# Kernel tuning notes

Hardware: AMD Instinct MI355X
Metric: run time of the kernel (lower is better)

## Reference

```python
import jax, jax.numpy as jnp
import numpy as np

N = 50000      # nodes
E = 800000     # edges (avg degree 16)
F = 128        # num_features
H = 128        # hidden_channels
C = 16         # num_classes
KEEP = 0.5     # dropout keep prob


def setup_inputs() -> dict:
    key = jax.random.key(0)
    ks = jax.random.split(key, 7)
    x = jax.random.normal(ks[0], (N, F), dtype=jnp.float32)
    edge_index = jax.random.randint(ks[1], (2, E), 0, N, dtype=jnp.int64)
    W1 = jax.random.normal(ks[2], (F, H), dtype=jnp.float32) / np.float32(np.sqrt(F))
    b1 = jnp.zeros((H,), dtype=jnp.float32)
    W2 = jax.random.normal(ks[3], (H, C), dtype=jnp.float32) / np.float32(np.sqrt(H))
    b2 = jnp.zeros((C,), dtype=jnp.float32)
    # deterministic dropout mask (train-mode dropout, prob=0.5), pre-scaled by 1/keep
    dropout_mask = (jax.random.uniform(ks[4], (N, H)) < KEEP).astype(jnp.float32) / np.float32(KEEP)
    return {"x": x, "edge_index": edge_index, "W1": W1, "b1": b1,
            "W2": W2, "b2": b2, "dropout_mask": dropout_mask}


def _gather_mean(h, src, dst, n_nodes):
    # irregular gather (h[src]) + segment scatter-add at dst, then mean by in-degree
    agg = jax.ops.segment_sum(h[src], dst, num_segments=n_nodes)  # [N, c]
    deg = jax.ops.segment_sum(jnp.ones_like(dst, dtype=h.dtype), dst, num_segments=n_nodes)
    return agg / jnp.maximum(deg, 1.0)[:, None]


def reference(x, edge_index, W1, b1, W2, b2, dropout_mask):
    src, dst = edge_index[0], edge_index[1]
    # linmaps1: 0th->1st order broadcast; identity for singleton reference domains
    h = _gather_mean(x, src, dst, N)          # ConvolutionalLayer_1P #1: gather
    h = h @ W1 + b1                           # linear transform
    h = jax.nn.relu(h)
    h = h * dropout_mask                      # Dropout(prob=0.5)
    h = _gather_mean(h, src, dst, N)          # ConvolutionalLayer_1P #2: gather
    out = h @ W2 + b2
    # linmaps0: 1st->0th order reduce; identity for singleton domains
    return out
```

## Files before the change

### kernel.cpp

```cpp
#include <hip/hip_runtime.h>

#define NNODES 50000
#define NEDGES 800000
#define FDIM 128
#define HDIM 128
#define CDIM 16

#define NBUCK 256
#define BCAP 6144
#define NBA 391

typedef __attribute__((ext_vector_type(8))) short bf16x8;
typedef __attribute__((ext_vector_type(4))) float f32x4;

__device__ __forceinline__ ushort f32_to_bf16_rne(float f) {
  unsigned u = __float_as_uint(f);
  unsigned rounded = u + 0x7fffu + ((u >> 16) & 1u);
  return (ushort)(rounded >> 16);
}
__device__ __forceinline__ float bf_lo(unsigned u) { return __uint_as_float(u << 16); }
__device__ __forceinline__ float bf_hi(unsigned u) { return __uint_as_float(u & 0xffff0000u); }

__global__ __launch_bounds__(256) void k_prep_binA(
    const int* __restrict__ src, const int* __restrict__ dst,
    int* __restrict__ gcur, unsigned* __restrict__ ebuf,
    const float* __restrict__ x, ushort* __restrict__ xh,
    const float* __restrict__ W1, ushort* __restrict__ W1T,
    const float* __restrict__ W2, ushort* __restrict__ W2T) {
  __shared__ int cnt[NBUCK];
  __shared__ int base[NBUCK];
  int tid = threadIdx.x;
  if (blockIdx.x < NBA) {
    int e0 = blockIdx.x * 2048;
    cnt[tid] = 0;
    __syncthreads();
    int sv[8], dv[8];
    #pragma unroll
    for (int i = 0; i < 8; ++i) {
      int e = e0 + i * 256 + tid;
      if (e < NEDGES) {
        sv[i] = src[e];
        dv[i] = dst[e];
        atomicAdd(&cnt[dv[i] >> 8], 1);
      } else {
        dv[i] = -1;
      }
    }
    __syncthreads();
    base[tid] = atomicAdd(&gcur[tid], cnt[tid]);
    cnt[tid] = 0;
    __syncthreads();
    #pragma unroll
    for (int i = 0; i < 8; ++i) {
      if (dv[i] >= 0) {
        int b = dv[i] >> 8;
        int pos = base[b] + atomicAdd(&cnt[b], 1);
        if (pos < BCAP)
          ebuf[b * BCAP + pos] = ((unsigned)(dv[i] & 255) << 16) | (unsigned)sv[i];
      }
    }
    return;
  }
  int t = (blockIdx.x - NBA) * 256 + tid;
  if (t < 1600000) {
    float4 v = *reinterpret_cast<const float4*>(&x[t * 4]);
    ushort4 o;
    o.x = f32_to_bf16_rne(v.x);
    o.y = f32_to_bf16_rne(v.y);
    o.z = f32_to_bf16_rne(v.z);
    o.w = f32_to_bf16_rne(v.w);
    *reinterpret_cast<ushort4*>(&xh[t * 4]) = o;
    return;
  }
  t -= 1600000;
  if (t < 16384) {
    int c = t >> 7, k = t & 127;
    W1T[c * 128 + k] = f32_to_bf16_rne(W1[k * 128 + c]);
    return;
  }
  t -= 16384;
  if (t < 2048) {
    int c = t >> 7, k = t & 127;
    W2T[c * 128 + k] = f32_to_bf16_rne(W2[k * 16 + c]);
  }
}

__global__ __launch_bounds__(256) void k_binB(
    const int* __restrict__ gcur, const unsigned* __restrict__ ebuf,
    int* __restrict__ deg, int* __restrict__ offs, ushort* __restrict__ ssrc) {
  __shared__ int s[NBUCK];
  __shared__ int doff[NBUCK];
  __shared__ int dcur[NBUCK];
  int tid = threadIdx.x;
  int b = blockIdx.x;

  int c = gcur[tid];
  if (c > BCAP) c = BCAP;
  s[tid] = c;
  for (int off = 1; off < 256; off <<= 1) {
    __syncthreads();
    int t = (tid >= off) ? s[tid - off] : 0;
    __syncthreads();
    s[tid] += t;
  }
  __syncthreads();
  int my_base = (b > 0) ? s[b - 1] : 0;
  int count = s[b] - my_base;

  dcur[tid] = 0;
  __syncthreads();
  const unsigned* eb = &ebuf[b * BCAP];
  for (int e = tid; e < count; e += 256) {
    atomicAdd(&dcur[eb[e] >> 16], 1);
  }
  __syncthreads();
  int dn = dcur[tid];
  s[tid] = dn;
  for (int off = 1; off < 256; off <<= 1) {
    __syncthreads();
    int t = (tid >= off) ? s[tid - off] : 0;
    __syncthreads();
    s[tid] += t;
  }
  __syncthreads();
  doff[tid] = s[tid] - dn;
  int node = b * 256 + tid;
  if (node < NNODES) {
    deg[node] = dn;
    offs[node] = my_base + doff[tid];
  }
  dcur[tid] = 0;
  __syncthreads();

  for (int e = tid; e < count; e += 256) {
    unsigned v = eb[e];
    int loc = v >> 16;
    int pos = my_base + doff[loc] + atomicAdd(&dcur[loc], 1);
    ssrc[pos] = (ushort)(v & 0xffffu);
  }
}

__global__ __launch_bounds__(256) void k_spmm1(
    const ushort* __restrict__ xh, const int* __restrict__ offs,
    const int* __restrict__ deg, const ushort* __restrict__ ssrc,
    ushort* __restrict__ aggh) {
  int tid = threadIdx.x;
  int grp = tid >> 4;
  int l16 = tid & 15;
  int n = blockIdx.x * 16 + grp;
  if (n >= NNODES) return;
  int start = offs[n];
  int d = deg[n];
  const ushort* base = xh + l16 * 8;
  float a0[8] = {0,0,0,0,0,0,0,0};
  float a1[8] = {0,0,0,0,0,0,0,0};
  float a2[8] = {0,0,0,0,0,0,0,0};
  float a3[8] = {0,0,0,0,0,0,0,0};
  int j = 0;
  for (; j + 3 < d; j += 4) {
    int s0 = ssrc[start + j + 0];
    int s1 = ssrc[start + j + 1];
    int s2 = ssrc[start + j + 2];
    int s3 = ssrc[start + j + 3];
    uint4 u0 = *reinterpret_cast<const uint4*>(base + s0 * FDIM);
    uint4 u1 = *reinterpret_cast<const uint4*>(base + s1 * FDIM);
    uint4 u2 = *reinterpret_cast<const uint4*>(base + s2 * FDIM);
    uint4 u3 = *reinterpret_cast<const uint4*>(base + s3 * FDIM);
    a0[0] += bf_lo(u0.x); a0[1] += bf_hi(u0.x); a0[2] += bf_lo(u0.y); a0[3] += bf_hi(u0.y);
    a0[4] += bf_lo(u0.z); a0[5] += bf_hi(u0.z); a0[6] += bf_lo(u0.w); a0[7] += bf_hi(u0.w);
    a1[0] += bf_lo(u1.x); a1[1] += bf_hi(u1.x); a1[2] += bf_lo(u1.y); a1[3] += bf_hi(u1.y);
    a1[4] += bf_lo(u1.z); a1[5] += bf_hi(u1.z); a1[6] += bf_lo(u1.w); a1[7] += bf_hi(u1.w);
    a2[0] += bf_lo(u2.x); a2[1] += bf_hi(u2.x); a2[2] += bf_lo(u2.y); a2[3] += bf_hi(u2.y);
    a2[4] += bf_lo(u2.z); a2[5] += bf_hi(u2.z); a2[6] += bf_lo(u2.w); a2[7] += bf_hi(u2.w);
    a3[0] += bf_lo(u3.x); a3[1] += bf_hi(u3.x); a3[2] += bf_lo(u3.y); a3[3] += bf_hi(u3.y);
    a3[4] += bf_lo(u3.z); a3[5] += bf_hi(u3.z); a3[6] += bf_lo(u3.w); a3[7] += bf_hi(u3.w);
  }
  for (; j < d; ++j) {
    int s0 = ssrc[start + j];
    uint4 u0 = *reinterpret_cast<const uint4*>(base + s0 * FDIM);
    a0[0] += bf_lo(u0.x); a0[1] += bf_hi(u0.x); a0[2] += bf_lo(u0.y); a0[3] += bf_hi(u0.y);
    a0[4] += bf_lo(u0.z); a0[5] += bf_hi(u0.z); a0[6] += bf_lo(u0.w); a0[7] += bf_hi(u0.w);
  }
  float inv = 1.0f / (float)(d > 0 ? d : 1);
  unsigned r[4];
  #pragma unroll
  for (int k = 0; k < 4; ++k) {
    float e0 = (a0[2 * k] + a1[2 * k] + a2[2 * k] + a3[2 * k]) * inv;
    float e1 = (a0[2 * k + 1] + a1[2 * k + 1] + a2[2 * k + 1] + a3[2 * k + 1]) * inv;
    r[k] = (unsigned)f32_to_bf16_rne(e0) | ((unsigned)f32_to_bf16_rne(e1) << 16);
  }
  uint4 o; o.x = r[0]; o.y = r[1]; o.z = r[2]; o.w = r[3];
  *reinterpret_cast<uint4*>(&aggh[(size_t)n * FDIM + l16 * 8]) = o;
}

#define HT_STRIDE 132
__global__ __launch_bounds__(256) void k_dense(
    const ushort* __restrict__ aggh, const ushort* __restrict__ W1T,
    const float* __restrict__ b1, const float* __restrict__ mask,
    const ushort* __restrict__ W2T, ushort* __restrict__ zh) {
  __shared__ ushort hT[4][16 * HT_STRIDE];
  int w = threadIdx.x >> 6;
  int lane = threadIdx.x & 63;
  int nw = blockIdx.x * 64 + w * 16;
  if (nw >= NNODES) return;
  int l15 = lane & 15, quad = lane >> 4;

  f32x4 acc[8];
  #pragma unroll
  for (int ct = 0; ct < 8; ++ct) acc[ct] = (f32x4){0.f, 0.f, 0.f, 0.f};

  const ushort* arow = &aggh[(size_t)(nw + l15) * 128 + quad * 8];
  #pragma unroll
  for (int kk = 0; kk < 4; ++kk) {
    bf16x8 a = *reinterpret_cast<const bf16x8*>(arow + kk * 32);
    #pragma unroll
    for (int ct = 0; ct < 8; ++ct) {
      bf16x8 b = *reinterpret_cast<const bf16x8*>(
          &W1T[(size_t)(ct * 16 + l15) * 128 + kk * 32 + quad * 8]);
      acc[ct] = __builtin_amdgcn_mfma_f32_16x16x32_bf16(a, b, acc[ct], 0, 0, 0);
    }
  }

  ushort* ht = hT[w];
  #pragma unroll
  for (int ct = 0; ct < 8; ++ct) {
    int col = ct * 16 + l15;
    float bb = b1[col];
    #pragma unroll
    for (int r = 0; r < 4; ++r) {
      int node = nw + quad * 4 + r;
      float v = acc[ct][r] + bb;
      v = v > 0.f ? v : 0.f;
      v *= mask[(size_t)node * 128 + col];
      ht[(quad * 4 + r) * HT_STRIDE + col] = f32_to_bf16_rne(v);
    }
  }

  f32x4 zacc = (f32x4){0.f, 0.f, 0.f, 0.f};
  #pragma unroll
  for (int kk = 0; kk < 4; ++kk) {
    const ushort* ap = &ht[l15 * HT_STRIDE + kk * 32 + quad * 8];
    ushort4 alo = *reinterpret_cast<const ushort4*>(ap);
    ushort4 ahi = *reinterpret_cast<const ushort4*>(ap + 4);
    bf16x8 a2 = (bf16x8){(short)alo.x, (short)alo.y, (short)alo.z, (short)alo.w,
                         (short)ahi.x, (short)ahi.y, (short)ahi.z, (short)ahi.w};
    bf16x8 b2 = *reinterpret_cast<const bf16x8*>(&W2T[l15 * 128 + kk * 32 + quad * 8]);
    zacc = __builtin_amdgcn_mfma_f32_16x16x32_bf16(a2, b2, zacc, 0, 0, 0);
  }
  #pragma unroll
  for (int r = 0; r < 4; ++r) {
    zh[(size_t)(nw + quad * 4 + r) * 16 + l15] = f32_to_bf16_rne(zacc[r]);
  }
}

__global__ void k_spmm2(const ushort* __restrict__ zh, const int* __restrict__ offs,
                        const int* __restrict__ deg, const ushort* __restrict__ ssrc,
                        const float* __restrict__ b2, float* __restrict__ out) {
  int tid = threadIdx.x;
  int nl = tid >> 4, c = tid & 15;
  int n = blockIdx.x * 8 + nl;
  if (n >= NNODES) return;
  int start = offs[n], d = deg[n];
  float a0 = 0.f, a1 = 0.f, a2 = 0.f, a3 = 0.f;
  int j = 0;
  for (; j + 3 < d; j += 4) {
    int s0 = ssrc[start + j + 0], s1 = ssrc[start + j + 1];
    int s2 = ssrc[start + j + 2], s3 = ssrc[start + j + 3];
    a0 += __uint_as_float((unsigned)zh[s0 * 16 + c] << 16);
    a1 += __uint_as_float((unsigned)zh[s1 * 16 + c] << 16);
    a2 += __uint_as_float((unsigned)zh[s2 * 16 + c] << 16);
    a3 += __uint_as_float((unsigned)zh[s3 * 16 + c] << 16);
  }
  for (; j < d; ++j) a0 += __uint_as_float((unsigned)zh[ssrc[start + j] * 16 + c] << 16);
  out[n * 16 + c] = (a0 + a1 + a2 + a3) / (float)(d > 0 ? d : 1) + b2[c];
}


extern "C" void kernel_launch(void* const* d_in, const int* in_sizes, int n_in,
                              void* d_out, int out_size, void* d_ws, size_t ws_size,
                              hipStream_t stream) {
  const float* x    = (const float*)d_in[0];
  const int*   ei   = (const int*)d_in[1];
  const float* W1   = (const float*)d_in[2];
  const float* b1   = (const float*)d_in[3];
  const float* W2   = (const float*)d_in[4];
  const float* b2   = (const float*)d_in[5];
  const float* mask = (const float*)d_in[6];
  float* out = (float*)d_out;

  const int* src = ei;
  const int* dst = ei + NEDGES;

  char* ws = (char*)d_ws;
  size_t o = 0;
  auto alloc = [&](size_t bytes) -> void* {
    void* p = ws + o;
    o += (bytes + 255) & ~(size_t)255;
    return p;
  };
  ushort*   aggh = (ushort*)alloc((size_t)NNODES * 128 * 2);
  ushort*   xh   = (ushort*)alloc((size_t)NNODES * 128 * 2);
  ushort*   zh   = (ushort*)alloc((size_t)NNODES * 16 * 2);
  ushort*   W1T  = (ushort*)alloc((size_t)128 * 128 * 2);
  ushort*   W2T  = (ushort*)alloc((size_t)16 * 128 * 2);
  int*      deg  = (int*)alloc((size_t)NNODES * 4);
  int*      offs = (int*)alloc((size_t)NNODES * 4);
  int*      gcur = (int*)alloc((size_t)NBUCK * 4);
  unsigned* ebuf = (unsigned*)alloc((size_t)NBUCK * BCAP * 4);
  ushort*   ssrc = (ushort*)alloc((size_t)NEDGES * 2);

  int prep_threads = 1600000 + 16384 + 2048;
  int prep_blocks = (prep_threads + 255) / 256;

  hipMemsetAsync(gcur, 0, NBUCK * sizeof(int), stream);
  k_prep_binA<<<NBA + prep_blocks, 256, 0, stream>>>(src, dst, gcur, ebuf,
                                                     x, xh, W1, W1T, W2, W2T);
  k_binB<<<NBUCK, 256, 0, stream>>>(gcur, ebuf, deg, offs, ssrc);
  k_spmm1<<<(NNODES + 15) / 16, 256, 0, stream>>>(xh, offs, deg, ssrc, aggh);
  k_dense<<<(NNODES + 63) / 64, 256, 0, stream>>>(aggh, W1T, b1, mask, W2T, zh);
  k_spmm2<<<(NNODES + 7) / 8, 128, 0, stream>>>(zh, offs, deg, ssrc, b2, out);
}
```

Measured before the change: 182.2 us.

## Split bf16 feature table into column quarters and gather per quarter with persistent blocks

The bf16 copy of x is stored as four column-quarter planes of 32 features each. The first gather kernel becomes a persistent kernel that claims tiles through an atomic counter and walks all node blocks for quarter 0 before moving to quarter 1, so each pass gathers from a 3.2 MB plane that can stay cache-resident. Each node now uses 4 lanes with 8 loads in flight, and the output stores are nontemporal. The cost is that the neighbour index list is read four times, plus per-tile atomics and barriers.

```diff
diff --git a/kernel.cpp b/kernel.cpp
--- a/kernel.cpp
+++ b/kernel.cpp
@@ -10,8 +10,14 @@
 #define BCAP 6144
 #define NBA 391
 
+#define NQ 4
+#define QBLK 64
+#define NT1 782
+#define NTILES (NQ * NT1)
+
 typedef __attribute__((ext_vector_type(8))) short bf16x8;
 typedef __attribute__((ext_vector_type(4))) float f32x4;
+typedef __attribute__((ext_vector_type(4))) unsigned u32x4;
 
 __device__ __forceinline__ ushort f32_to_bf16_rne(float f) {
   unsigned u = __float_as_uint(f);
@@ -69,7 +75,11 @@
     o.y = f32_to_bf16_rne(v.y);
     o.z = f32_to_bf16_rne(v.z);
     o.w = f32_to_bf16_rne(v.w);
-    *reinterpret_cast<ushort4*>(&xh[t * 4]) = o;
+    int e0 = t * 4;
+    int n = e0 >> 7;
+    int c = e0 & 127;
+    int idx = ((c >> 5) * NNODES + n) * 32 + (c & 31);
+    *reinterpret_cast<ushort4*>(&xh[idx]) = o;
     return;
   }
   t -= 1600000;
@@ -140,57 +150,71 @@
   }
 }
 
+#define ACC8(U) do { \
+    acc[0] += bf_lo(U.x); acc[1] += bf_hi(U.x); \
+    acc[2] += bf_lo(U.y); acc[3] += bf_hi(U.y); \
+    acc[4] += bf_lo(U.z); acc[5] += bf_hi(U.z); \
+    acc[6] += bf_lo(U.w); acc[7] += bf_hi(U.w); } while (0)
+
 __global__ __launch_bounds__(256) void k_spmm1(
     const ushort* __restrict__ xh, const int* __restrict__ offs,
     const int* __restrict__ deg, const ushort* __restrict__ ssrc,
-    ushort* __restrict__ aggh) {
+    int* __restrict__ tctr, ushort* __restrict__ aggh) {
+  __shared__ int s_tile;
   int tid = threadIdx.x;
-  int grp = tid >> 4;
-  int l16 = tid & 15;
-  int n = blockIdx.x * 16 + grp;
-  if (n >= NNODES) return;
-  int start = offs[n];
-  int d = deg[n];
-  const ushort* base = xh + l16 * 8;
-  float a0[8] = {0,0,0,0,0,0,0,0};
-  float a1[8] = {0,0,0,0,0,0,0,0};
-  float a2[8] = {0,0,0,0,0,0,0,0};
-  float a3[8] = {0,0,0,0,0,0,0,0};
-  int j = 0;
-  for (; j + 3 < d; j += 4) {
-    int s0 = ssrc[start + j + 0];
-    int s1 = ssrc[start + j + 1];
-    int s2 = ssrc[start + j + 2];
-    int s3 = ssrc[start + j + 3];
-    uint4 u0 = *reinterpret_cast<const uint4*>(base + s0 * FDIM);
-    uint4 u1 = *reinterpret_cast<const uint4*>(base + s1 * FDIM);
-    uint4 u2 = *reinterpret_cast<const uint4*>(base + s2 * FDIM);
-    uint4 u3 = *reinterpret_cast<const uint4*>(base + s3 * FDIM);
-    a0[0] += bf_lo(u0.x); a0[1] += bf_hi(u0.x); a0[2] += bf_lo(u0.y); a0[3] += bf_hi(u0.y);
-    a0[4] += bf_lo(u0.z); a0[5] += bf_hi(u0.z); a0[6] += bf_lo(u0.w); a0[7] += bf_hi(u0.w);
-    a1[0] += bf_lo(u1.x); a1[1] += bf_hi(u1.x); a1[2] += bf_lo(u1.y); a1[3] += bf_hi(u1.y);
-    a1[4] += bf_lo(u1.z); a1[5] += bf_hi(u1.z); a1[6] += bf_lo(u1.w); a1[7] += bf_hi(u1.w);
-    a2[0] += bf_lo(u2.x); a2[1] += bf_hi(u2.x); a2[2] += bf_lo(u2.y); a2[3] += bf_hi(u2.y);
-    a2[4] += bf_lo(u2.z); a2[5] += bf_hi(u2.z); a2[6] += bf_lo(u2.w); a2[7] += bf_hi(u2.w);
-    a3[0] += bf_lo(u3.x); a3[1] += bf_hi(u3.x); a3[2] += bf_lo(u3.y); a3[3] += bf_hi(u3.y);
-    a3[4] += bf_lo(u3.z); a3[5] += bf_hi(u3.z); a3[6] += bf_lo(u3.w); a3[7] += bf_hi(u3.w);
-  }
-  for (; j < d; ++j) {
-    int s0 = ssrc[start + j];
-    uint4 u0 = *reinterpret_cast<const uint4*>(base + s0 * FDIM);
-    a0[0] += bf_lo(u0.x); a0[1] += bf_hi(u0.x); a0[2] += bf_lo(u0.y); a0[3] += bf_hi(u0.y);
-    a0[4] += bf_lo(u0.z); a0[5] += bf_hi(u0.z); a0[6] += bf_lo(u0.w); a0[7] += bf_hi(u0.w);
-  }
-  float inv = 1.0f / (float)(d > 0 ? d : 1);
-  unsigned r[4];
-  #pragma unroll
-  for (int k = 0; k < 4; ++k) {
-    float e0 = (a0[2 * k] + a1[2 * k] + a2[2 * k] + a3[2 * k]) * inv;
-    float e1 = (a0[2 * k + 1] + a1[2 * k + 1] + a2[2 * k + 1] + a3[2 * k + 1]) * inv;
-    r[k] = (unsigned)f32_to_bf16_rne(e0) | ((unsigned)f32_to_bf16_rne(e1) << 16);
-  }
-  uint4 o; o.x = r[0]; o.y = r[1]; o.z = r[2]; o.w = r[3];
-  *reinterpret_cast<uint4*>(&aggh[(size_t)n * FDIM + l16 * 8]) = o;
+  int grp = tid >> 2;
+  int l4 = tid & 3;
+  for (;;) {
+    if (tid == 0) s_tile = atomicAdd(tctr, 1);
+    __syncthreads();
+    int tile = s_tile;
+    __syncthreads();
+    if (tile >= NTILES) break;
+    int q = tile / NT1;
+    int nb = tile - q * NT1;
+    int n = nb * QBLK + grp;
+    if (n < NNODES) {
+      int start = offs[n];
+      int d = deg[n];
+      const ushort* xq = xh + (size_t)q * NNODES * 32 + l4 * 8;
+      float acc[8] = {0, 0, 0, 0, 0, 0, 0, 0};
+      int j = 0;
+      for (; j + 7 < d; j += 8) {
+        int s0 = ssrc[start + j + 0];
+        int s1 = ssrc[start + j + 1];
+        int s2 = ssrc[start + j + 2];
+        int s3 = ssrc[start + j + 3];
+        int s4 = ssrc[start + j + 4];
+        int s5 = ssrc[start + j + 5];
+        int s6 = ssrc[start + j + 6];
+        int s7 = ssrc[start + j + 7];
+        uint4 u0 = *reinterpret_cast<const uint4*>(xq + ((size_t)s0 << 5));
+        uint4 u1 = *reinterpret_cast<const uint4*>(xq + ((size_t)s1 << 5));
+        uint4 u2 = *reinterpret_cast<const uint4*>(xq + ((size_t)s2 << 5));
+        uint4 u3 = *reinterpret_cast<const uint4*>(xq + ((size_t)s3 << 5));
+        uint4 u4 = *reinterpret_cast<const uint4*>(xq + ((size_t)s4 << 5));
+        uint4 u5 = *reinterpret_cast<const uint4*>(xq + ((size_t)s5 << 5));
+        uint4 u6 = *reinterpret_cast<const uint4*>(xq + ((size_t)s6 << 5));
+        uint4 u7 = *reinterpret_cast<const uint4*>(xq + ((size_t)s7 << 5));
+        ACC8(u0); ACC8(u1); ACC8(u2); ACC8(u3);
+        ACC8(u4); ACC8(u5); ACC8(u6); ACC8(u7);
+      }
+      for (; j < d; ++j) {
+        int s0 = ssrc[start + j];
+        uint4 u0 = *reinterpret_cast<const uint4*>(xq + ((size_t)s0 << 5));
+        ACC8(u0);
+      }
+      float inv = 1.0f / (float)(d > 0 ? d : 1);
+      u32x4 o;
+      #pragma unroll
+      for (int k = 0; k < 4; ++k) {
+        o[k] = (unsigned)f32_to_bf16_rne(acc[2 * k] * inv) |
+               ((unsigned)f32_to_bf16_rne(acc[2 * k + 1] * inv) << 16);
+      }
+      __builtin_nontemporal_store(
+          o, reinterpret_cast<u32x4*>(&aggh[(size_t)n * 128 + q * 32 + l4 * 8]));
+    }
+  }
 }
 
 #define HT_STRIDE 132
@@ -272,7 +296,8 @@
     a3 += __uint_as_float((unsigned)zh[s3 * 16 + c] << 16);
   }
   for (; j < d; ++j) a0 += __uint_as_float((unsigned)zh[ssrc[start + j] * 16 + c] << 16);
-  out[n * 16 + c] = (a0 + a1 + a2 + a3) / (float)(d > 0 ? d : 1) + b2[c];
+  float v = (a0 + a1 + a2 + a3) / (float)(d > 0 ? d : 1) + b2[c];
+  __builtin_nontemporal_store(v, &out[n * 16 + c]);
 }
 
 
@@ -305,18 +330,19 @@
   ushort*   W2T  = (ushort*)alloc((size_t)16 * 128 * 2);
   int*      deg  = (int*)alloc((size_t)NNODES * 4);
   int*      offs = (int*)alloc((size_t)NNODES * 4);
-  int*      gcur = (int*)alloc((size_t)NBUCK * 4);
+  int*      gcur = (int*)alloc((size_t)(NBUCK + 4) * 4);
   unsigned* ebuf = (unsigned*)alloc((size_t)NBUCK * BCAP * 4);
   ushort*   ssrc = (ushort*)alloc((size_t)NEDGES * 2);
+  int*      tctr = gcur + NBUCK;
 
   int prep_threads = 1600000 + 16384 + 2048;
   int prep_blocks = (prep_threads + 255) / 256;
 
-  hipMemsetAsync(gcur, 0, NBUCK * sizeof(int), stream);
+  hipMemsetAsync(gcur, 0, (NBUCK + 4) * sizeof(int), stream);
   k_prep_binA<<<NBA + prep_blocks, 256, 0, stream>>>(src, dst, gcur, ebuf,
                                                      x, xh, W1, W1T, W2, W2T);
   k_binB<<<NBUCK, 256, 0, stream>>>(gcur, ebuf, deg, offs, ssrc);
-  k_spmm1<<<(NNODES + 15) / 16, 256, 0, stream>>>(xh, offs, deg, ssrc, aggh);
+  k_spmm1<<<NT1, 256, 0, stream>>>(xh, offs, deg, ssrc, tctr, aggh);
   k_dense<<<(NNODES + 63) / 64, 256, 0, stream>>>(aggh, W1T, b1, mask, W2T, zh);
   k_spmm2<<<(NNODES + 7) / 8, 128, 0, stream>>>(zh, offs, deg, ssrc, b2, out);
 }
```

Result: slower. 209.7 us (+15.1%).
